# Performance work log

Measured on AMD Instinct MI355X. Metric: run time of the kernel, lower is better.

## Reference

```python
import jax, jax.numpy as jnp
import numpy as np
import math

EPS = 1e-9
NORM = 1.0 / math.sqrt(20.0)  # num_neighbours=20 default


def _mixing(x1, x2, B, W, b):
    # nn.Bilinear (no bias): x_bi[n,k] = sum_ij x1[n,i] B[k,i,j] x2[n,j]
    x_bi = jnp.einsum('ni,kij->nkj', x1, B)
    x_bi = jnp.einsum('nkj,nj->nk', x_bi, x2)
    x = jnp.concatenate([x1, x2, x_bi], axis=-1)
    return x @ W.T + b


def _rowstd(x):
    # torch.std default: unbiased (ddof=1)
    return jnp.std(x, axis=1, ddof=1, keepdims=True)


def setup_inputs() -> dict:
    key = jax.random.key(0)
    N, E = 100000, 2000000
    DN, DE, DA_N, DA_E = 32, 32, 3, 1
    ks = jax.random.split(key, 24)

    def nrm(k, shape, fan_in):
        return jax.random.normal(k, shape, dtype=jnp.float32) / np.sqrt(fan_in)

    inp = {
        'xn': jax.random.normal(ks[0], (N, DN), dtype=jnp.float32),
        'xn_attr': jax.random.normal(ks[1], (N, DA_N), dtype=jnp.float32),
        'xe_attr': jax.random.normal(ks[2], (E, DA_E), dtype=jnp.float32),
        'xe_src': jax.random.randint(ks[3], (E,), 0, N),
        'xe_dst': jax.random.randint(ks[4], (E,), 0, N),
        # fc1: Linear(1, xe_dim); fc2: Linear(1, xn_dim)
        'W_fc1': nrm(ks[5], (DE, 1), 1), 'b_fc1': jnp.zeros((DE,), jnp.float32),
        'W_fc2': nrm(ks[6], (DN, 1), 1), 'b_fc2': jnp.zeros((DN,), jnp.float32),
        # mix_xn: Mixing(DN, DA_N, DN)
        'B_mix_xn': nrm(ks[7], (DN, DN, DA_N), DN * DA_N),
        'W_mix_xn': nrm(ks[8], (DN, 2 * DN + DA_N), 2 * DN + DA_N),
        'b_mix_xn': jnp.zeros((DN,), jnp.float32),
        # nodes_to_edges.mix: Mixing(DN, DN, DN)
        'B_n2e': nrm(ks[9], (DN, DN, DN), DN * DN),
        'W_n2e': nrm(ks[10], (DN, 3 * DN), 3 * DN),
        'b_n2e': jnp.zeros((DN,), jnp.float32),
        # mix_xe: Mixing(DE, DA_E, DE)
        'B_mix_xe': nrm(ks[11], (DE, DE, DA_E), DE * DA_E),
        'W_mix_xe': nrm(ks[12], (DE, 2 * DE + DA_E), 2 * DE + DA_E),
        'b_mix_xe': jnp.zeros((DE,), jnp.float32),
        # edges_to_nodes.mix: Mixing(DE, DE, DE)
        'B_e2n': nrm(ks[13], (DE, DE, DE), DE * DE),
        'W_e2n': nrm(ks[14], (DE, 3 * DE), 3 * DE),
        'b_e2n': jnp.zeros((DE,), jnp.float32),
    }
    return inp


def reference(xn, xn_attr, xe_attr, xe_src, xe_dst,
              W_fc1, b_fc1, W_fc2, b_fc2,
              B_mix_xn, W_mix_xn, b_mix_xn,
              B_n2e, W_n2e, b_n2e,
              B_mix_xe, W_mix_xe, b_mix_xe,
              B_e2n, W_e2n, b_e2n):
    n_nodes = xn.shape[0]
    # node mixing + per-row std norm
    xn = _mixing(xn, xn_attr, B_mix_xn, W_mix_xn, b_mix_xn)
    xn = xn / (_rowstd(xn) + EPS)
    # fc1 weight: [E, xe_dim]
    w1 = jax.nn.silu(xe_attr @ W_fc1.T + b_fc1)
    # NodesToEdges: gather -> grad/ave -> mixing
    xg, xd = xn[xe_src], xn[xe_dst]
    xe = _mixing(w1 * (xg - xd), w1 * (xg + xd) * 0.5, B_n2e, W_n2e, b_n2e)
    xe = _mixing(xe, xe_attr, B_mix_xe, W_mix_xe, b_mix_xe)
    xe = xe / (_rowstd(xe) + EPS)
    # fc2 weight: [E, xn_dim]
    w2 = jax.nn.silu(xe_attr @ W_fc2.T + b_fc2)
    # EdgesToNodes: scatter-add over dst/src, diff/sum, mixing
    wxe = w2 * xe
    xn1 = jax.ops.segment_sum(wxe, xe_dst, num_segments=n_nodes) * NORM
    xn2 = jax.ops.segment_sum(wxe, xe_src, num_segments=n_nodes) * NORM
    xn = _mixing(xn1 - xn2, xn1 + xn2, B_e2n, W_e2n, b_e2n)
    xn = jax.nn.silu(xn)
    xn = xn / (_rowstd(xn) + EPS)
    return xn
```

## Files before the change

### kernel.cpp

```cpp
#include <hip/hip_runtime.h>
#include <hip/hip_bf16.h>

#define N_NODES 100000
#define N_EDGES 2000000
#define EPS 1e-9f
#define NORMC 0.22360679774997896f

#define BKSZ   512
#define NBK1   196
#define NBK    392
#define NSB    512
#define CE     3907
#define NITEMS 4000000

typedef short s8 __attribute__((ext_vector_type(8)));
typedef float f4 __attribute__((ext_vector_type(4)));

__device__ __forceinline__ float silu_f(float x) {
    return x / (1.0f + __expf(-x));
}

__device__ __forceinline__ ushort f2bfu(float f) {
    union { __hip_bfloat16 b; ushort u; } cv;
    cv.b = __float2bfloat16(f);
    return cv.u;
}

__device__ __forceinline__ uint pkbf(float lo, float hi) {
    float2 t; t.x = lo; t.y = hi;
    union { __hip_bfloat162 b; uint u; } cv;
    cv.b = __float22bfloat162_rn(t);
    return cv.u;
}


__device__ float mext(const float* __restrict__ W, const float* __restrict__ B,
                      const float* __restrict__ bias, int n, int i, int j) {
    if (i < 32 && j < 32) {
        float r = 0.f;
        #pragma unroll
        for (int m = 0; m < 32; ++m) r += W[n*96 + 64 + m] * B[m*1024 + i*32 + j];
        return r;
    }
    if (i < 32) return W[n*96 + i];
    if (j < 32) return W[n*96 + 32 + j];
    return bias[n];
}

__global__ void prep_kernel(const float* __restrict__ W_n2e, const float* __restrict__ B_n2e,
                            const float* __restrict__ b_n2e,
                            const float* __restrict__ W_e2n, const float* __restrict__ B_e2n,
                            const float* __restrict__ b_e2n,
                            const float* __restrict__ W_mix_xn, const float* __restrict__ B_mix_xn,
                            const float* __restrict__ b_mix_xn,
                            const float* __restrict__ W_mix_xe, const float* __restrict__ B_mix_xe,
                            const float* __restrict__ b_mix_xe,
                            ushort* __restrict__ MF, ushort* __restrict__ MG,
                            float* __restrict__ BpN, float* __restrict__ WxE,
                            float* __restrict__ CtE) {
    int t = blockIdx.x * blockDim.x + threadIdx.x;
    if (t < 69632) {
        int u = (t < 34816) ? t : t - 34816;
        int tt = u & 7, lane = (u >> 3) & 63, rest = u >> 9;
        int nt = rest & 1, kk = rest >> 1;
        int n = nt*16 + (lane & 15);
        int kl = ((lane >> 4) & 3) * 8 + tt;
        int i, j;
        if (kk < 33) { i = kk; j = kl; } else { i = kl; j = 32; }
        if (t < 34816) MF[u] = f2bfu(mext(W_n2e, B_n2e, b_n2e, n, i, j));
        else           MG[u] = f2bfu(mext(W_e2n, B_e2n, b_e2n, n, i, j));
    } else if (t < 73856) {
        int u = t - 69632;
        int k = u & 31, ij = u >> 5;
        int i = ij >> 2, j = ij & 3;
        float r;
        if (i < 32 && j < 3) {
            r = 0.f;
            #pragma unroll
            for (int m = 0; m < 32; ++m) r += W_mix_xn[k*67 + 35 + m] * B_mix_xn[m*96 + i*3 + j];
        } else if (i < 32 && j == 3) {
            r = W_mix_xn[k*67 + i];
        } else if (i == 32 && j < 3) {
            r = W_mix_xn[k*67 + 32 + j];
        } else {
            r = b_mix_xn[k];
        }
        BpN[ij*32 + k] = r;
    } else if (t < 74912) {
        int u = t - 73856;
        int k = u & 31, i = u >> 5;
        WxE[i*32 + k] = (i < 32) ? W_mix_xe[k*65 + i] : b_mix_xe[k];
    } else if (t < 75968) {
        int u = t - 74912;
        int k = u & 31, i = u >> 5;
        float r;
        if (i < 32) {
            r = 0.f;
            #pragma unroll
            for (int m = 0; m < 32; ++m) r += W_mix_xe[k*65 + 33 + m] * B_mix_xe[m*32 + i];
        } else {
            r = W_mix_xe[k*65 + 32];
        }
        CtE[i*32 + k] = r;
    }
}

__global__ void zero_kernel(float4* __restrict__ p, int n4) {
    int i = blockIdx.x * blockDim.x + threadIdx.x;
    int stride = gridDim.x * blockDim.x;
    float4 z = {0.f, 0.f, 0.f, 0.f};
    for (; i < n4; i += stride) p[i] = z;
}

__global__ __launch_bounds__(256) void node_kernel(
    const float* __restrict__ xn, const float* __restrict__ xn_attr,
    const float* __restrict__ BpN, float* __restrict__ xn_norm) {
    int n = blockIdx.x * 256 + threadIdx.x;
    if (n >= N_NODES) return;
    float x[33];
    const float4* xr = (const float4*)(xn + (size_t)n * 32);
    #pragma unroll
    for (int q = 0; q < 8; ++q) {
        float4 v = xr[q];
        x[q*4+0] = v.x; x[q*4+1] = v.y; x[q*4+2] = v.z; x[q*4+3] = v.w;
    }
    x[32] = 1.f;
    float at[4];
    at[0] = xn_attr[n*3]; at[1] = xn_attr[n*3+1]; at[2] = xn_attr[n*3+2]; at[3] = 1.f;

    float acc[32];
    #pragma unroll
    for (int k = 0; k < 32; ++k) acc[k] = 0.f;
    #pragma unroll
    for (int i = 0; i < 33; ++i) {
        #pragma unroll
        for (int j = 0; j < 4; ++j) {
            float s = x[i] * at[j];
            const float* bp = BpN + (i*4 + j) * 32;
            #pragma unroll
            for (int k = 0; k < 32; ++k) acc[k] = fmaf(bp[k], s, acc[k]);
        }
    }
    float mean = 0.f;
    #pragma unroll
    for (int k = 0; k < 32; ++k) mean += acc[k];
    mean *= (1.0f / 32.0f);
    float var = 0.f;
    #pragma unroll
    for (int k = 0; k < 32; ++k) { float d = acc[k] - mean; var += d * d; }
    var *= (1.0f / 31.0f);
    float inv = 1.0f / (sqrtf(var) + EPS);
    float4* out = (float4*)(xn_norm + (size_t)n * 32);
    #pragma unroll
    for (int q = 0; q < 8; ++q) {
        float4 v;
        v.x = acc[q*4+0]*inv; v.y = acc[q*4+1]*inv; v.z = acc[q*4+2]*inv; v.w = acc[q*4+3]*inv;
        out[q] = v;
    }
}


__global__ __launch_bounds__(256) void count_kernel(
    const int* __restrict__ xe_src, const int* __restrict__ xe_dst,
    int* __restrict__ cntg) {
    __shared__ int cnt[NBK];
    int tid = threadIdx.x, b = blockIdx.x;
    for (int k = tid; k < NBK; k += 256) cnt[k] = 0;
    __syncthreads();
    int e0 = b * CE;
    for (int i = tid; i < CE; i += 256) {
        int e = e0 + i;
        if (e < N_EDGES) {
            atomicAdd(&cnt[xe_dst[e] >> 9], 1);
            atomicAdd(&cnt[NBK1 + (xe_src[e] >> 9)], 1);
        }
    }
    __syncthreads();
    for (int k = tid; k < NBK; k += 256) cntg[k * NSB + b] = cnt[k];
}

__global__ __launch_bounds__(1024) void scan_kernel(
    const int* __restrict__ cntg, int* __restrict__ scang) {
    __shared__ int part[1024];
    int t = threadIdx.x;
    const int CHUNK = 196;
    int base = t * CHUNK;
    int s = 0;
    for (int i = 0; i < CHUNK; ++i) s += cntg[base + i];
    part[t] = s;
    __syncthreads();
    for (int off = 1; off < 1024; off <<= 1) {
        int v = part[t];
        int add = (t >= off) ? part[t - off] : 0;
        __syncthreads();
        part[t] = v + add;
        __syncthreads();
    }
    int run = (t == 0) ? 0 : part[t - 1];
    for (int i = 0; i < CHUNK; ++i) {
        int c = cntg[base + i];
        scang[base + i] = run;
        run += c;
    }
}

__global__ __launch_bounds__(256) void scatter_kernel(
    const int* __restrict__ xe_src, const int* __restrict__ xe_dst,
    const int* __restrict__ scang, int* __restrict__ bucketed) {
    __shared__ int cur[NBK];
    int tid = threadIdx.x, b = blockIdx.x;
    for (int k = tid; k < NBK; k += 256) cur[k] = scang[k * NSB + b];
    __syncthreads();
    int e0 = b * CE;
    for (int i = tid; i < CE; i += 256) {
        int e = e0 + i;
        if (e < N_EDGES) {
            int d = xe_dst[e];
            int p = atomicAdd(&cur[d >> 9], 1);
            bucketed[p] = e | ((d & 511) << 21);
            int s_ = xe_src[e];
            p = atomicAdd(&cur[NBK1 + (s_ >> 9)], 1);
            bucketed[p] = e | ((s_ & 511) << 21);
        }
    }
}

__global__ __launch_bounds__(256) void gather_kernel(
    const ushort* __restrict__ wxe, const int* __restrict__ bucketed,
    const int* __restrict__ scang, float* __restrict__ sd0) {
    __shared__ float accs[BKSZ * 33];
    int tid = threadIdx.x, bk = blockIdx.x;
    for (int i = tid; i < BKSZ * 33; i += 256) accs[i] = 0.f;
    __syncthreads();
    int start = scang[bk * NSB];
    int end = (bk == NBK - 1) ? NITEMS : scang[(bk + 1) * NSB];
    for (int i = start + tid; i < end; i += 256) {
        int p = bucketed[i];
        int e = p & 0x1FFFFF;
        int ln = (p >> 21) & 511;
        const uint4* wp = (const uint4*)(wxe + (size_t)e * 32);
        float* ap = &accs[ln * 33];
        #pragma unroll
        for (int q = 0; q < 4; ++q) {
            uint4 w = wp[q];
            uint uu[4] = {w.x, w.y, w.z, w.w};
            #pragma unroll
            for (int c = 0; c < 4; ++c) {
                uint u = uu[c];
                float lo = __uint_as_float((u & 0xFFFFu) << 16);
                float hi = __uint_as_float(u & 0xFFFF0000u);
                int k = q * 8 + c * 2;
                atomicAdd(&ap[k], lo);
                atomicAdd(&ap[k + 1], hi);
            }
        }
    }
    __syncthreads();
    int side = (bk < NBK1) ? 0 : 1;
    int nb = side ? bk - NBK1 : bk;
    float* out = sd0 + (size_t)side * 3211264 + (size_t)nb * BKSZ * 32;
    for (int i = tid; i < BKSZ * 32; i += 256) {
        int node = i >> 5, k = i & 31;
        out[i] = accs[node * 33 + k];
    }
}


__device__ __forceinline__ void gemm33(const ushort* __restrict__ sM,
                                       float* __restrict__ a_f,
                                       const ushort* __restrict__ ab,
                                       const float* __restrict__ biasv, int tid) {
    int lane = tid & 63, wv = tid >> 6;
    int m = lane & 15, h = lane >> 4;
    int base = wv * 64;
    float bfv[4][8];
    s8 araw[4];
    #pragma unroll
    for (int g = 0; g < 4; ++g) {
        const ushort* rp = &ab[(size_t)(base + g*16 + m) * 72];
        union { s8 v; ushort s[8]; } braw;
        braw.v = *(const s8*)&rp[h*8];
        #pragma unroll
        for (int t = 0; t < 8; ++t) {
            union { uint u; float f; } cv; cv.u = ((uint)braw.s[t]) << 16;
            bfv[g][t] = cv.f;
        }
        araw[g] = *(const s8*)&rp[32 + h*8];
    }
    f4 c[4][2];
    #pragma unroll
    for (int g = 0; g < 4; ++g) {
        c[g][0] = (f4){0.f, 0.f, 0.f, 0.f};
        c[g][1] = (f4){0.f, 0.f, 0.f, 0.f};
    }
    const s8* M8 = (const s8*)sM;
    #pragma unroll
    for (int kk = 0; kk < 33; ++kk) {
        s8 mf0 = M8[(kk*2 + 0)*64 + lane];
        s8 mf1 = M8[(kk*2 + 1)*64 + lane];
        #pragma unroll
        for (int g = 0; g < 4; ++g) {
            float as = a_f[(size_t)(base + g*16 + m) * 33 + kk];
            union { s8 v; uint u[4]; } af;
            #pragma unroll
            for (int t = 0; t < 4; ++t) af.u[t] = pkbf(as * bfv[g][2*t], as * bfv[g][2*t+1]);
            c[g][0] = __builtin_amdgcn_mfma_f32_16x16x32_bf16(af.v, mf0, c[g][0], 0, 0, 0);
            c[g][1] = __builtin_amdgcn_mfma_f32_16x16x32_bf16(af.v, mf1, c[g][1], 0, 0, 0);
        }
    }
    {
        s8 mf0 = M8[66*64 + lane];
        s8 mf1 = M8[67*64 + lane];
        #pragma unroll
        for (int g = 0; g < 4; ++g) {
            c[g][0] = __builtin_amdgcn_mfma_f32_16x16x32_bf16(araw[g], mf0, c[g][0], 0, 0, 0);
            c[g][1] = __builtin_amdgcn_mfma_f32_16x16x32_bf16(araw[g], mf1, c[g][1], 0, 0, 0);
        }
    }
    float b0 = biasv[m], b1 = biasv[16 + m];
    #pragma unroll
    for (int g = 0; g < 4; ++g) {
        int rowb = base + g*16 + h*4;
        #pragma unroll
        for (int r = 0; r < 4; ++r) {
            a_f[(size_t)(rowb + r) * 33 + m]      = c[g][0][r] + b0;
            a_f[(size_t)(rowb + r) * 33 + 16 + m] = c[g][1][r] + b1;
        }
    }
}

#define TILES_E 7813

template<bool STORE>
__global__ __launch_bounds__(256, 1) void edge_kernel(
    const float* __restrict__ xn_norm, const float* __restrict__ xe_attr,
    const int* __restrict__ xe_src, const int* __restrict__ xe_dst,
    const float* __restrict__ W_fc1, const float* __restrict__ b_fc1,
    const float* __restrict__ W_fc2, const float* __restrict__ b_fc2,
    const ushort* __restrict__ MF, const float* __restrict__ biasE,
    const float* __restrict__ WxE, const float* __restrict__ CtE,
    float* __restrict__ acc1, float* __restrict__ acc2,
    ushort* __restrict__ wxe) {
    __shared__ __align__(16) ushort sM[34816];
    __shared__ __align__(16) float  a_f[256 * 33];
    __shared__ __align__(16) ushort ab[256 * 72];
    int tid = threadIdx.x;
    {
        const float4* s4p = (const float4*)MF;
        float4* d4p = (float4*)sM;
        #pragma unroll
        for (int i = 0; i < 17; ++i) d4p[tid + i*256] = s4p[tid + i*256];
    }
    uint* ab32 = (uint*)ab;

    int t = blockIdx.x;
    float attrP = 0.f; int srcP = 0, dstP = 0; bool okP = false;
    float4 gP[8], dP[8];
    {
        int e = t*256 + tid;
        okP = e < N_EDGES;
        int ec = okP ? e : 0;
        attrP = xe_attr[ec]; srcP = xe_src[ec]; dstP = xe_dst[ec];
        const float4* gp = (const float4*)(xn_norm + (size_t)srcP * 32);
        const float4* dp = (const float4*)(xn_norm + (size_t)dstP * 32);
        #pragma unroll
        for (int q = 0; q < 8; ++q) { gP[q] = gp[q]; dP[q] = dp[q]; }
    }

    for (; t < TILES_E; t += 256) {
        float attr = attrP; int csrc = srcP, cdst = dstP; bool okC = okP;
        float vs = okC ? 1.f : 0.f;
        #pragma unroll
        for (int q = 0; q < 8; ++q) {
            float4 g = gP[q], d = dP[q];
            float gg[4] = {g.x, g.y, g.z, g.w};
            float dd[4] = {d.x, d.y, d.z, d.w};
            #pragma unroll
            for (int p = 0; p < 2; ++p) {
                int k = q*4 + p*2;
                float w0 = silu_f(attr * W_fc1[k]   + b_fc1[k])   * vs;
                float w1 = silu_f(attr * W_fc1[k+1] + b_fc1[k+1]) * vs;
                float av0 = w0 * (gg[2*p]   - dd[2*p]);
                float av1 = w1 * (gg[2*p+1] - dd[2*p+1]);
                float bv0 = w0 * (gg[2*p]   + dd[2*p])   * 0.5f;
                float bv1 = w1 * (gg[2*p+1] + dd[2*p+1]) * 0.5f;
                a_f[tid*33 + k]   = av0;
                a_f[tid*33 + k+1] = av1;
                ab32[tid*36 + (k>>1)]      = pkbf(bv0, bv1);
                ab32[tid*36 + 16 + (k>>1)] = pkbf(av0, av1);
            }
        }
        a_f[tid*33 + 32] = 1.f;

        int tn = t + 256;
        if (tn < TILES_E) {
            int e = tn*256 + tid;
            okP = e < N_EDGES;
            int ec = okP ? e : 0;
            attrP = xe_attr[ec]; srcP = xe_src[ec]; dstP = xe_dst[ec];
            const float4* gp = (const float4*)(xn_norm + (size_t)srcP * 32);
            const float4* dp = (const float4*)(xn_norm + (size_t)dstP * 32);
            #pragma unroll
            for (int q = 0; q < 8; ++q) { gP[q] = gp[q]; dP[q] = dp[q]; }
        }
        __syncthreads();

        gemm33(sM, a_f, ab, biasE, tid);
        __syncthreads();

        float2 y2[16];
        #pragma unroll
        for (int k2 = 0; k2 < 16; ++k2) y2[k2] = make_float2(0.f, 0.f);
        for (int i = 0; i < 33; ++i) {
            float xi = a_f[tid*33 + i];
            const float2* wx2 = (const float2*)(WxE + i * 32);
            const float2* ct2 = (const float2*)(CtE + i * 32);
            #pragma unroll
            for (int k2 = 0; k2 < 16; ++k2) {
                float2 w = wx2[k2], ctv = ct2[k2];
                float lx = fmaf(attr, ctv.x, w.x);
                float ly = fmaf(attr, ctv.y, w.y);
                y2[k2].x = fmaf(lx, xi, y2[k2].x);
                y2[k2].y = fmaf(ly, xi, y2[k2].y);
            }
        }
        float mean = 0.f;
        #pragma unroll
        for (int k2 = 0; k2 < 16; ++k2) mean += y2[k2].x + y2[k2].y;
        mean *= (1.0f / 32.0f);
        float var = 0.f;
        #pragma unroll
        for (int k2 = 0; k2 < 16; ++k2) {
            float dx = y2[k2].x - mean, dy = y2[k2].y - mean;
            var += dx*dx + dy*dy;
        }
        var *= (1.0f / 31.0f);
        float inv = 1.0f / (sqrtf(var) + EPS);

        if (okC) {
            if (STORE) {
                uint pkv[16];
                #pragma unroll
                for (int k2 = 0; k2 < 16; ++k2) {
                    float w20 = silu_f(attr * W_fc2[2*k2]   + b_fc2[2*k2]);
                    float w21 = silu_f(attr * W_fc2[2*k2+1] + b_fc2[2*k2+1]);
                    pkv[k2] = pkbf(w20 * y2[k2].x * inv, w21 * y2[k2].y * inv);
                }
                uint4* wp = (uint4*)(wxe + (size_t)(t*256 + tid) * 32);
                #pragma unroll
                for (int q = 0; q < 4; ++q) {
                    uint4 v; v.x = pkv[q*4]; v.y = pkv[q*4+1]; v.z = pkv[q*4+2]; v.w = pkv[q*4+3];
                    wp[q] = v;
                }
            } else {
                float* p1 = acc1 + (size_t)cdst * 32;
                float* p2 = acc2 + (size_t)csrc * 32;
                #pragma unroll
                for (int k = 0; k < 32; ++k) {
                    float yk = (k & 1) ? y2[k>>1].y : y2[k>>1].x;
                    float w2 = silu_f(attr * W_fc2[k] + b_fc2[k]);
                    float v = w2 * yk * inv;
                    unsafeAtomicAdd(p1 + k, v);
                    unsafeAtomicAdd(p2 + k, v);
                }
            }
        }
    }
}

#define TILES_F 391

__global__ __launch_bounds__(256, 1) void final_kernel(
    const float* __restrict__ acc1, const float* __restrict__ acc2,
    const ushort* __restrict__ MG, const float* __restrict__ biasG,
    float* __restrict__ out) {
    __shared__ __align__(16) ushort sM[34816];
    __shared__ __align__(16) float  a_f[256 * 33];
    __shared__ __align__(16) ushort ab[256 * 72];
    int tid = threadIdx.x;
    {
        const float4* s4p = (const float4*)MG;
        float4* d4p = (float4*)sM;
        #pragma unroll
        for (int i = 0; i < 17; ++i) d4p[tid + i*256] = s4p[tid + i*256];
    }
    uint* ab32 = (uint*)ab;

    for (int t = blockIdx.x; t < TILES_F; t += 256) {
        int n = t*256 + tid;
        bool ok = n < N_NODES;
        int nn = ok ? n : 0;
        float vs = ok ? 1.f : 0.f;
        const float4* p1 = (const float4*)(acc1 + (size_t)nn * 32);
        const float4* p2 = (const float4*)(acc2 + (size_t)nn * 32);
        #pragma unroll
        for (int q = 0; q < 8; ++q) {
            float4 u1 = p1[q], u2 = p2[q];
            float a1[4] = {u1.x, u1.y, u1.z, u1.w};
            float a2[4] = {u2.x, u2.y, u2.z, u2.w};
            #pragma unroll
            for (int p = 0; p < 2; ++p) {
                int k = q*4 + p*2;
                float dv0 = (a1[2*p]   - a2[2*p])   * NORMC * vs;
                float dv1 = (a1[2*p+1] - a2[2*p+1]) * NORMC * vs;
                float sv0 = (a1[2*p]   + a2[2*p])   * NORMC * vs;
                float sv1 = (a1[2*p+1] + a2[2*p+1]) * NORMC * vs;
                a_f[tid*33 + k]   = dv0;
                a_f[tid*33 + k+1] = dv1;
                ab32[tid*36 + (k>>1)]      = pkbf(sv0, sv1);
                ab32[tid*36 + 16 + (k>>1)] = pkbf(dv0, dv1);
            }
        }
        a_f[tid*33 + 32] = 1.f;
        __syncthreads();

        gemm33(sM, a_f, ab, biasG, tid);
        __syncthreads();

        if (ok) {
            float z[32];
            float mean = 0.f;
            #pragma unroll
            for (int k = 0; k < 32; ++k) { z[k] = silu_f(a_f[tid*33 + k]); mean += z[k]; }
            mean *= (1.0f / 32.0f);
            float var = 0.f;
            #pragma unroll
            for (int k = 0; k < 32; ++k) { float d = z[k] - mean; var += d * d; }
            var *= (1.0f / 31.0f);
            float inv = 1.0f / (sqrtf(var) + EPS);
            float4* op = (float4*)(out + (size_t)n * 32);
            #pragma unroll
            for (int q = 0; q < 8; ++q) {
                float4 v;
                v.x = z[q*4+0]*inv; v.y = z[q*4+1]*inv; v.z = z[q*4+2]*inv; v.w = z[q*4+3]*inv;
                op[q] = v;
            }
        }
    }
}

extern "C" void kernel_launch(void* const* d_in, const int* in_sizes, int n_in,
                              void* d_out, int out_size, void* d_ws, size_t ws_size,
                              hipStream_t stream) {
    const float* xn       = (const float*)d_in[0];
    const float* xn_attr  = (const float*)d_in[1];
    const float* xe_attr  = (const float*)d_in[2];
    const int*   xe_src   = (const int*)d_in[3];
    const int*   xe_dst   = (const int*)d_in[4];
    const float* W_fc1    = (const float*)d_in[5];
    const float* b_fc1    = (const float*)d_in[6];
    const float* W_fc2    = (const float*)d_in[7];
    const float* b_fc2    = (const float*)d_in[8];
    const float* B_mix_xn = (const float*)d_in[9];
    const float* W_mix_xn = (const float*)d_in[10];
    const float* b_mix_xn = (const float*)d_in[11];
    const float* B_n2e    = (const float*)d_in[12];
    const float* W_n2e    = (const float*)d_in[13];
    const float* b_n2e    = (const float*)d_in[14];
    const float* B_mix_xe = (const float*)d_in[15];
    const float* W_mix_xe = (const float*)d_in[16];
    const float* b_mix_xe = (const float*)d_in[17];
    const float* B_e2n    = (const float*)d_in[18];
    const float* W_e2n    = (const float*)d_in[19];
    const float* b_e2n    = (const float*)d_in[20];

    float* ws = (float*)d_ws;
    const size_t MAIN_BYTES = 46065088ULL * 4ULL;
    bool big = ws_size >= MAIN_BYTES;

    if (big) {
        float*  xn_norm = ws;
        float*  sd0     = ws + 3200000;
        float*  sd1     = ws + 6411264;
        ushort* MF      = (ushort*)(ws + 9622528);
        ushort* MG      = MF + 34816;
        float*  BpN     = ws + 9657344;
        float*  WxE     = ws + 9661568;
        float*  CtE     = ws + 9662624;
        ushort* wxe     = (ushort*)(ws + 9663680);
        int*    bucketed= (int*)(ws + 41663680);
        int*    cntg    = (int*)(ws + 45663680);
        int*    scang   = (int*)(ws + 45864384);

        prep_kernel<<<297, 256, 0, stream>>>(W_n2e, B_n2e, b_n2e, W_e2n, B_e2n, b_e2n,
                                             W_mix_xn, B_mix_xn, b_mix_xn,
                                             W_mix_xe, B_mix_xe, b_mix_xe,
                                             MF, MG, BpN, WxE, CtE);
        node_kernel<<<391, 256, 0, stream>>>(xn, xn_attr, BpN, xn_norm);
        count_kernel<<<NSB, 256, 0, stream>>>(xe_src, xe_dst, cntg);
        scan_kernel<<<1, 1024, 0, stream>>>(cntg, scang);
        scatter_kernel<<<NSB, 256, 0, stream>>>(xe_src, xe_dst, scang, bucketed);
        edge_kernel<true><<<256, 256, 0, stream>>>(xn_norm, xe_attr, xe_src, xe_dst,
                                                   W_fc1, b_fc1, W_fc2, b_fc2,
                                                   MF, b_n2e, WxE, CtE,
                                                   nullptr, nullptr, wxe);
        gather_kernel<<<NBK, 256, 0, stream>>>(wxe, bucketed, scang, sd0);
        final_kernel<<<391, 256, 0, stream>>>(sd0, sd1, MG, b_e2n, (float*)d_out);
    } else {
        float*  xn_norm = ws;
        float*  acc1    = ws + 3200000;
        float*  acc2    = ws + 6400000;
        ushort* MF      = (ushort*)(ws + 9600000);
        ushort* MG      = MF + 34816;
        float*  BpN     = ws + 9600000 + 34816;
        float*  WxE     = BpN + 4224;
        float*  CtE     = WxE + 1056;

        prep_kernel<<<297, 256, 0, stream>>>(W_n2e, B_n2e, b_n2e, W_e2n, B_e2n, b_e2n,
                                             W_mix_xn, B_mix_xn, b_mix_xn,
                                             W_mix_xe, B_mix_xe, b_mix_xe,
                                             MF, MG, BpN, WxE, CtE);
        zero_kernel<<<2048, 256, 0, stream>>>((float4*)acc1, 1600000);
        node_kernel<<<391, 256, 0, stream>>>(xn, xn_attr, BpN, xn_norm);
        edge_kernel<false><<<256, 256, 0, stream>>>(xn_norm, xe_attr, xe_src, xe_dst,
                                                    W_fc1, b_fc1, W_fc2, b_fc2,
                                                    MF, b_n2e, WxE, CtE,
                                                    acc1, acc2, nullptr);
        final_kernel<<<391, 256, 0, stream>>>(acc1, acc2, MG, b_e2n, (float*)d_out);
    }
}
```

Before: 1.728 ms.

## Halve node bucket size and split each edge row across four lanes with prefetch

Node buckets shrink from 512 to 256 nodes, which doubles the number of gather blocks (782) and halves their shared accumulator footprint. The scan gains bounds guards because the count table no longer divides evenly into 1024×196 chunks. In the gather, four threads now share each edge: each loads one 16-byte quarter of the bf16 row. Bucket indices and rows are software-pipelined two steps ahead to hide global latency. The risk is more shared-atomic contention per bucket and more count/scan bookkeeping.

```diff
diff --git a/kernel.cpp b/kernel.cpp
--- a/kernel.cpp
+++ b/kernel.cpp
@@ -6,11 +6,11 @@
 #define EPS 1e-9f
 #define NORMC 0.22360679774997896f
 
-#define BKSZ   512
-#define NBK1   196
-#define NBK    392
-#define NSB    512
-#define CE     3907
+#define BKSZ   256
+#define NBK1   391
+#define NBK    782
+#define NSB    256
+#define CE     7813
 #define NITEMS 4000000
 
 typedef short s8 __attribute__((ext_vector_type(8)));
@@ -171,13 +171,15 @@
     for (int i = tid; i < CE; i += 256) {
         int e = e0 + i;
         if (e < N_EDGES) {
-            atomicAdd(&cnt[xe_dst[e] >> 9], 1);
-            atomicAdd(&cnt[NBK1 + (xe_src[e] >> 9)], 1);
+            atomicAdd(&cnt[xe_dst[e] >> 8], 1);
+            atomicAdd(&cnt[NBK1 + (xe_src[e] >> 8)], 1);
         }
     }
     __syncthreads();
     for (int k = tid; k < NBK; k += 256) cntg[k * NSB + b] = cnt[k];
 }
+
+#define SCAN_TOT (NBK * NSB)
 
 __global__ __launch_bounds__(1024) void scan_kernel(
     const int* __restrict__ cntg, int* __restrict__ scang) {
@@ -186,7 +188,10 @@
     const int CHUNK = 196;
     int base = t * CHUNK;
     int s = 0;
-    for (int i = 0; i < CHUNK; ++i) s += cntg[base + i];
+    for (int i = 0; i < CHUNK; ++i) {
+        int idx = base + i;
+        if (idx < SCAN_TOT) s += cntg[idx];
+    }
     part[t] = s;
     __syncthreads();
     for (int off = 1; off < 1024; off <<= 1) {
@@ -198,9 +203,12 @@
     }
     int run = (t == 0) ? 0 : part[t - 1];
     for (int i = 0; i < CHUNK; ++i) {
-        int c = cntg[base + i];
-        scang[base + i] = run;
-        run += c;
+        int idx = base + i;
+        if (idx < SCAN_TOT) {
+            int c = cntg[idx];
+            scang[idx] = run;
+            run += c;
+        }
     }
 }
 
@@ -216,11 +224,11 @@
         int e = e0 + i;
         if (e < N_EDGES) {
             int d = xe_dst[e];
-            int p = atomicAdd(&cur[d >> 9], 1);
-            bucketed[p] = e | ((d & 511) << 21);
+            int p = atomicAdd(&cur[d >> 8], 1);
+            bucketed[p] = e | ((d & 255) << 21);
             int s_ = xe_src[e];
-            p = atomicAdd(&cur[NBK1 + (s_ >> 9)], 1);
-            bucketed[p] = e | ((s_ & 511) << 21);
+            p = atomicAdd(&cur[NBK1 + (s_ >> 8)], 1);
+            bucketed[p] = e | ((s_ & 255) << 21);
         }
     }
 }
@@ -234,26 +242,29 @@
     __syncthreads();
     int start = scang[bk * NSB];
     int end = (bk == NBK - 1) ? NITEMS : scang[(bk + 1) * NSB];
-    for (int i = start + tid; i < end; i += 256) {
-        int p = bucketed[i];
-        int e = p & 0x1FFFFF;
-        int ln = (p >> 21) & 511;
-        const uint4* wp = (const uint4*)(wxe + (size_t)e * 32);
-        float* ap = &accs[ln * 33];
-        #pragma unroll
-        for (int q = 0; q < 4; ++q) {
-            uint4 w = wp[q];
-            uint uu[4] = {w.x, w.y, w.z, w.w};
-            #pragma unroll
-            for (int c = 0; c < 4; ++c) {
-                uint u = uu[c];
-                float lo = __uint_as_float((u & 0xFFFFu) << 16);
-                float hi = __uint_as_float(u & 0xFFFF0000u);
-                int k = q * 8 + c * 2;
-                atomicAdd(&ap[k], lo);
-                atomicAdd(&ap[k + 1], hi);
-            }
-        }
+    int q = tid >> 2, g = tid & 3;
+    uint4 z4; z4.x = 0u; z4.y = 0u; z4.z = 0u; z4.w = 0u;
+
+    int i0 = start + q;
+    int p0 = (i0 < end) ? bucketed[i0] : 0;
+    int p1 = (i0 + 64 < end) ? bucketed[i0 + 64] : 0;
+    uint4 r0 = (i0 < end)
+             ? *(const uint4*)(wxe + (size_t)(p0 & 0x1FFFFF) * 32 + g * 8) : z4;
+
+    for (int i = i0; i < end; i += 64) {
+        int pn = (i + 128 < end) ? bucketed[i + 128] : 0;
+        uint4 r1 = (i + 64 < end)
+                 ? *(const uint4*)(wxe + (size_t)(p1 & 0x1FFFFF) * 32 + g * 8) : z4;
+        int ln = (p0 >> 21) & 255;
+        float* ap = &accs[ln * 33 + g * 8];
+        uint uu[4] = {r0.x, r0.y, r0.z, r0.w};
+        #pragma unroll
+        for (int c = 0; c < 4; ++c) {
+            uint u = uu[c];
+            atomicAdd(&ap[c*2],     __uint_as_float((u & 0xFFFFu) << 16));
+            atomicAdd(&ap[c*2 + 1], __uint_as_float(u & 0xFFFF0000u));
+        }
+        p0 = p1; p1 = pn; r0 = r1;
     }
     __syncthreads();
     int side = (bk < NBK1) ? 0 : 1;
```

Result: slower. 2.013 ms (+16.5%).
